# Optimization experiments

Hardware: AMD Instinct MI355X
Metric: run time of the kernel (lower is better)

Reference implementation:

```python
import jax, jax.numpy as jnp
import numpy as np

B, T, C = 32, 2048, 64
H, N = 1, 64            # head_size = n_embd -> single head of size 64 (CUDA assert: C//H == 64)
LAYER_ID, N_LAYER = 1, 4
TMIX_DIM, TDEC_DIM = 32, 64
LN_EPS = 1e-5 * 8**2


def setup_inputs() -> dict:
    key = jax.random.key(0)
    ks = jax.random.split(key, 10)
    r01 = LAYER_ID / (N_LAYER - 1)          # ratio_0_to_1
    r10 = 1.0 - LAYER_ID / N_LAYER          # ratio_1_to_almost0
    ddd = (jnp.arange(C, dtype=jnp.float32) / C)[None, None, :]   # (1,1,C)
    tm_x = 1.0 - ddd**r10
    tm_w = 1.0 - ddd**r10
    tm_k = 1.0 - ddd**r10
    tm_v = 1.0 - (ddd**r10 + 0.3 * r01)
    tm_r = 1.0 - ddd**(0.5 * r10)
    tm_g = 1.0 - ddd**(0.5 * r10)
    unif = lambda k, s: jax.random.uniform(k, s, minval=-1e-4, maxval=1e-4, dtype=jnp.float32)
    maa_w1 = unif(ks[0], (C, TMIX_DIM * 5))
    maa_w2 = unif(ks[1], (5, TMIX_DIM, C))
    n = jnp.arange(C, dtype=jnp.float32)
    t_decay = (-6.0 + 5.0 * (n / (C - 1))**(0.7 + 1.3 * r01))[None, None, :]   # (1,1,C)
    dec_w1 = unif(ks[2], (C, TDEC_DIM))
    dec_w2 = unif(ks[3], (TDEC_DIM, C))
    zig = ((n + 1) % 3 - 1) * 0.1
    u = (r01 * (1.0 - n / (C - 1)) + zig).reshape(H, N)            # time_faaaa
    wscale = 0.02
    Wr = jax.random.normal(ks[4], (C, C), jnp.float32) * wscale
    Wk = jax.random.normal(ks[5], (C, C), jnp.float32) * wscale
    Wv = jax.random.normal(ks[6], (C, C), jnp.float32) * wscale
    Wg = jax.random.normal(ks[7], (C, C), jnp.float32) * wscale
    Wo = jax.random.normal(ks[8], (C, C), jnp.float32) * wscale
    ln_w = jnp.ones((C,), jnp.float32)
    ln_b = jnp.zeros((C,), jnp.float32)
    x = jax.random.normal(ks[9], (B, T, C), jnp.float32)
    return dict(x=x, tm_x=tm_x, tm_w=tm_w, tm_k=tm_k, tm_v=tm_v, tm_r=tm_r, tm_g=tm_g,
                maa_w1=maa_w1, maa_w2=maa_w2, t_decay=t_decay, dec_w1=dec_w1, dec_w2=dec_w2,
                u=u, Wr=Wr, Wk=Wk, Wv=Wv, Wg=Wg, Wo=Wo, ln_w=ln_w, ln_b=ln_b)


def _tmix(x, tm_x, tm_w, tm_k, tm_v, tm_r, tm_g, maa_w1, maa_w2, t_decay,
          dec_w1, dec_w2, u, Wr, Wk, Wv, Wg, Wo, ln_w, ln_b):
    # token shift: xx[t] = x[t-1] - x[t], x[-1] := 0
    xx = jnp.pad(x, ((0, 0), (1, 0), (0, 0)))[:, :-1] - x
    xxx = x + xx * tm_x
    a = jnp.tanh(xxx @ maa_w1).reshape(B, T, 5, TMIX_DIM)
    mw, mk, mv, mr, mg = jnp.einsum('btfk,fkc->fbtc', a, maa_w2)
    xw = x + xx * (tm_w + mw)
    xk = x + xx * (tm_k + mk)
    xv = x + xx * (tm_v + mv)
    xr = x + xx * (tm_r + mr)
    xg = x + xx * (tm_g + mg)
    r = xr @ Wr.T
    k = xk @ Wk.T
    v = xv @ Wv.T
    g = jax.nn.silu(xg @ Wg.T)
    w = t_decay + jnp.tanh(xw @ dec_w1) @ dec_w2
    dec = jnp.exp(-jnp.exp(w))               # data-dependent per-channel decay in (0,1)

    # WKV6 recurrence, time-major (T,B,H,N)
    hm = lambda t: t.reshape(B, T, H, N).transpose(1, 0, 2, 3)
    rT, kT, vT, dT = hm(r), hm(k), hm(v), hm(dec)

    def step(S, inp):
        rt, kt, vt, dt = inp                 # each (B,H,N)
        kv = kt[..., :, None] * vt[..., None, :]            # (B,H,N,N)
        y = jnp.einsum('bhi,bhij->bhj', rt, S + u[None, :, :, None] * kv)
        S = S * dt[..., :, None] + kv
        return S, y

    S0 = jnp.zeros((B, H, N, N), x.dtype)
    _, yT = jax.lax.scan(step, S0, (rT, kT, vT, dT))
    y = yT.transpose(1, 0, 2, 3).reshape(B, T, C)

    # GroupNorm over (B*T, C) with H groups, eps = 1e-5 * 64
    yg = y.reshape(B, T, H, N)
    mu = yg.mean(-1, keepdims=True)
    var = yg.var(-1, keepdims=True)
    yn = ((yg - mu) * jax.lax.rsqrt(var + LN_EPS)).reshape(B, T, C) * ln_w + ln_b
    return (yn * g) @ Wo.T


def reference(x, tm_x, tm_w, tm_k, tm_v, tm_r, tm_g, maa_w1, maa_w2, t_decay,
              dec_w1, dec_w2, u, Wr, Wk, Wv, Wg, Wo, ln_w, ln_b):
    return _tmix(x, tm_x, tm_w, tm_k, tm_v, tm_r, tm_g, maa_w1, maa_w2, t_decay,
                 dec_w1, dec_w2, u, Wr, Wk, Wv, Wg, Wo, ln_w, ln_b)
```

## Files before the change

### kernel.cpp

```cpp
#include <hip/hip_runtime.h>

#define BB 32
#define TT 2048
#define CC 64
#define BT (BB * TT)
#define NCH 64
#define CL 32
#define GN_EPS (1e-5f * 64.f)
#define SW 36
#define SA 68

typedef short short8 __attribute__((ext_vector_type(8)));
typedef float f32x4 __attribute__((ext_vector_type(4)));

__device__ __forceinline__ float rl(float v, int lane) {
  return __uint_as_float(__builtin_amdgcn_readlane(__float_as_uint(v), lane));
}
__device__ __forceinline__ float tanh_f(float x) {
  x = fminf(fmaxf(x, -10.f), 10.f);
  const float e = __expf(2.f * x);
  return (e - 1.f) / (e + 1.f);
}

__device__ __forceinline__ unsigned short f2bf(float x) {
  unsigned int u = __float_as_uint(x);
  u += 0x7FFFu + ((u >> 16) & 1u);
  return (unsigned short)(u >> 16);
}
__device__ __forceinline__ float bf2f(unsigned short h) {
  return __uint_as_float(((unsigned int)h) << 16);
}
__device__ __forceinline__ short8 cvt8(const float4 a, const float4 b) {
  short8 h;
  h[0] = (short)f2bf(a.x); h[1] = (short)f2bf(a.y);
  h[2] = (short)f2bf(a.z); h[3] = (short)f2bf(a.w);
  h[4] = (short)f2bf(b.x); h[5] = (short)f2bf(b.y);
  h[6] = (short)f2bf(b.z); h[7] = (short)f2bf(b.w);
  return h;
}
__device__ __forceinline__ short8 ldb8(const float* __restrict__ p) {
  const float4 v0 = *reinterpret_cast<const float4*>(p);
  const float4 v1 = *reinterpret_cast<const float4*>(p + 4);
  return cvt8(v0, v1);
}
__device__ __forceinline__ short8 ldb8_lds(const float* p) {
  const float4 v0 = *reinterpret_cast<const float4*>(p);
  const float4 v1 = *reinterpret_cast<const float4*>(p + 4);
  return cvt8(v0, v1);
}
__device__ __forceinline__ void splitload(const float* p, short8& h8, short8& l8) {
  const float4 v0 = *reinterpret_cast<const float4*>(p);
  const float4 v1 = *reinterpret_cast<const float4*>(p + 4);
  const float vv[8] = {v0.x, v0.y, v0.z, v0.w, v1.x, v1.y, v1.z, v1.w};
#pragma unroll
  for (int e = 0; e < 8; ++e) {
    const unsigned short hb = f2bf(vv[e]);
    h8[e] = (short)hb;
    l8[e] = (short)f2bf(vv[e] - bf2f(hb));
  }
}
__device__ __forceinline__ f32x4 mfma3(short8 ah, short8 al, short8 bh, short8 bl, f32x4 a) {
  a = __builtin_amdgcn_mfma_f32_16x16x32_bf16(ah, bh, a, 0, 0, 0);
  a = __builtin_amdgcn_mfma_f32_16x16x32_bf16(ah, bl, a, 0, 0, 0);
  a = __builtin_amdgcn_mfma_f32_16x16x32_bf16(al, bh, a, 0, 0, 0);
  return a;
}

__global__ __launch_bounds__(256) void preT_kernel(
    const float* __restrict__ maa_w1, const float* __restrict__ maa_w2,
    const float* __restrict__ dec_w1, const float* __restrict__ dec_w2,
    float* __restrict__ w1T, float* __restrict__ w2T,
    float* __restrict__ d1T, float* __restrict__ d2T)
{
  const int t0 = blockIdx.x * 256 + threadIdx.x;
  const int stride = gridDim.x * 256;
  for (int i = t0; i < 160 * 64; i += stride) {
    const int n = i >> 6, c = i & 63;
    w1T[i] = maa_w1[c * 160 + n];
  }
  for (int i = t0; i < 5 * 64 * 32; i += stride) {
    const int f = i >> 11, rem = i & 2047, n = rem >> 5, q = rem & 31;
    w2T[i] = maa_w2[(f * 32 + q) * 64 + n];
  }
  for (int i = t0; i < 4096; i += stride) {
    const int n = i >> 6, c = i & 63;
    d1T[i] = dec_w1[c * 64 + n];
    d2T[i] = dec_w2[c * 64 + n];
  }
}

#define LDS_A 36
#define LDS_X 68
__global__ __launch_bounds__(256) void mix_mfma_kernel(
    const float* __restrict__ x,
    const float* __restrict__ tm_x, const float* __restrict__ tm_w, const float* __restrict__ tm_k,
    const float* __restrict__ tm_v, const float* __restrict__ tm_r, const float* __restrict__ tm_g,
    const float* __restrict__ w1T, const float* __restrict__ w2T,
    const float* __restrict__ d1T, const float* __restrict__ d2T,
    const float* __restrict__ t_decay,
    float* __restrict__ xk_o, float* __restrict__ xv_o,
    float* __restrict__ xr_o, float* __restrict__ xg_o,
    float* __restrict__ rkdc)
{
  __shared__ float aT[4][32][LDS_A];
  __shared__ float xT[4][32][LDS_X];
  const int lane = threadIdx.x & 63;
  const int wid = threadIdx.x >> 6;
  const int col = lane & 15, half = lane >> 4;
  const int tok0 = blockIdx.x * 128 + wid * 32;

  short8 xa[2][2];
#pragma unroll
  for (int m = 0; m < 2; ++m)
#pragma unroll
    for (int kk = 0; kk < 2; ++kk) {
      const int tok = tok0 + m * 16 + col;
      const int kb = kk * 32 + half * 8;
      const float* pc = x + (size_t)tok * CC + kb;
      const float4 c0 = *reinterpret_cast<const float4*>(pc);
      const float4 c1 = *reinterpret_cast<const float4*>(pc + 4);
      float4 p0 = {0.f, 0.f, 0.f, 0.f}, p1 = {0.f, 0.f, 0.f, 0.f};
      if ((tok & (TT - 1)) != 0) {
        p0 = *reinterpret_cast<const float4*>(pc - CC);
        p1 = *reinterpret_cast<const float4*>(pc - CC + 4);
      }
      const float4 t0 = *reinterpret_cast<const float4*>(tm_x + kb);
      const float4 t1 = *reinterpret_cast<const float4*>(tm_x + kb + 4);
      const float cv[8] = {c0.x, c0.y, c0.z, c0.w, c1.x, c1.y, c1.z, c1.w};
      const float pv[8] = {p0.x, p0.y, p0.z, p0.w, p1.x, p1.y, p1.z, p1.w};
      const float tv[8] = {t0.x, t0.y, t0.z, t0.w, t1.x, t1.y, t1.z, t1.w};
      short8 h;
#pragma unroll
      for (int e = 0; e < 8; ++e)
        h[e] = (short)f2bf(fmaf(pv[e] - cv[e], tv[e], cv[e]));
      xa[m][kk] = h;
    }

  float xcv[2][4][4], xxv[2][4][4];
#pragma unroll
  for (int m = 0; m < 2; ++m)
#pragma unroll
    for (int reg = 0; reg < 4; ++reg) {
      const int tok = tok0 + m * 16 + half * 4 + reg;
      const bool has = (tok & (TT - 1)) != 0;
#pragma unroll
      for (int nt = 0; nt < 4; ++nt) {
        const size_t o = (size_t)tok * CC + nt * 16 + col;
        const float cur = x[o];
        const float prv = has ? x[o - CC] : 0.f;
        xcv[m][nt][reg] = cur;
        xxv[m][nt][reg] = prv - cur;
      }
    }

  auto process_f = [&](int f, const float* __restrict__ tmf,
                       float* __restrict__ gout) {
    f32x4 acc1[2][2];
#pragma unroll
    for (int m = 0; m < 2; ++m)
#pragma unroll
      for (int ntf = 0; ntf < 2; ++ntf) acc1[m][ntf] = (f32x4){0.f, 0.f, 0.f, 0.f};
    short8 b1[2][2];
#pragma unroll
    for (int ntf = 0; ntf < 2; ++ntf)
#pragma unroll
      for (int kk = 0; kk < 2; ++kk)
        b1[ntf][kk] = ldb8(w1T + (size_t)(f * 32 + ntf * 16 + col) * 64 + kk * 32 + half * 8);
#pragma unroll
    for (int m = 0; m < 2; ++m)
#pragma unroll
      for (int ntf = 0; ntf < 2; ++ntf)
#pragma unroll
        for (int kk = 0; kk < 2; ++kk)
          acc1[m][ntf] = __builtin_amdgcn_mfma_f32_16x16x32_bf16(
              xa[m][kk], b1[ntf][kk], acc1[m][ntf], 0, 0, 0);
#pragma unroll
    for (int m = 0; m < 2; ++m)
#pragma unroll
      for (int ntf = 0; ntf < 2; ++ntf)
#pragma unroll
        for (int reg = 0; reg < 4; ++reg)
          aT[wid][m * 16 + half * 4 + reg][ntf * 16 + col] = tanh_f(acc1[m][ntf][reg]);
    short8 a2[2];
#pragma unroll
    for (int m = 0; m < 2; ++m)
      a2[m] = ldb8_lds(&aT[wid][m * 16 + col][half * 8]);
    f32x4 acc2[2][4];
#pragma unroll
    for (int m = 0; m < 2; ++m)
#pragma unroll
      for (int nt = 0; nt < 4; ++nt) acc2[m][nt] = (f32x4){0.f, 0.f, 0.f, 0.f};
    short8 b2[4];
#pragma unroll
    for (int nt = 0; nt < 4; ++nt)
      b2[nt] = ldb8(w2T + (size_t)f * 2048 + (nt * 16 + col) * 32 + half * 8);
#pragma unroll
    for (int m = 0; m < 2; ++m)
#pragma unroll
      for (int nt = 0; nt < 4; ++nt)
        acc2[m][nt] = __builtin_amdgcn_mfma_f32_16x16x32_bf16(
            a2[m], b2[nt], acc2[m][nt], 0, 0, 0);
    float tmf4[4];
#pragma unroll
    for (int nt = 0; nt < 4; ++nt) tmf4[nt] = tmf[nt * 16 + col];
#pragma unroll
    for (int m = 0; m < 2; ++m)
#pragma unroll
      for (int nt = 0; nt < 4; ++nt)
#pragma unroll
        for (int reg = 0; reg < 4; ++reg) {
          const float val = fmaf(xxv[m][nt][reg], tmf4[nt] + acc2[m][nt][reg],
                                 xcv[m][nt][reg]);
          if (gout)
            gout[(size_t)(tok0 + m * 16 + half * 4 + reg) * CC + nt * 16 + col] = val;
          else
            xT[wid][m * 16 + half * 4 + reg][nt * 16 + col] = val;
        }
  };

  process_f(1, tm_k, xk_o);
  process_f(2, tm_v, xv_o);
  process_f(3, tm_r, xr_o);
  process_f(4, tm_g, xg_o);
  process_f(0, tm_w, nullptr);

  short8 xwf[2][2];
#pragma unroll
  for (int m = 0; m < 2; ++m)
#pragma unroll
    for (int kk = 0; kk < 2; ++kk)
      xwf[m][kk] = ldb8_lds(&xT[wid][m * 16 + col][kk * 32 + half * 8]);
  f32x4 hcc[2][4];
#pragma unroll
  for (int m = 0; m < 2; ++m)
#pragma unroll
    for (int nt = 0; nt < 4; ++nt) hcc[m][nt] = (f32x4){0.f, 0.f, 0.f, 0.f};
  short8 bd[4][2];
#pragma unroll
  for (int nt = 0; nt < 4; ++nt)
#pragma unroll
    for (int kk = 0; kk < 2; ++kk)
      bd[nt][kk] = ldb8(d1T + (size_t)(nt * 16 + col) * 64 + kk * 32 + half * 8);
#pragma unroll
  for (int m = 0; m < 2; ++m)
#pragma unroll
    for (int nt = 0; nt < 4; ++nt)
#pragma unroll
      for (int kk = 0; kk < 2; ++kk)
        hcc[m][nt] = __builtin_amdgcn_mfma_f32_16x16x32_bf16(
            xwf[m][kk], bd[nt][kk], hcc[m][nt], 0, 0, 0);
#pragma unroll
  for (int m = 0; m < 2; ++m)
#pragma unroll
    for (int nt = 0; nt < 4; ++nt)
#pragma unroll
      for (int reg = 0; reg < 4; ++reg)
        xT[wid][m * 16 + half * 4 + reg][nt * 16 + col] = tanh_f(hcc[m][nt][reg]);
  short8 hf[2][2];
#pragma unroll
  for (int m = 0; m < 2; ++m)
#pragma unroll
    for (int kk = 0; kk < 2; ++kk)
      hf[m][kk] = ldb8_lds(&xT[wid][m * 16 + col][kk * 32 + half * 8]);
  f32x4 wfa[2][4];
#pragma unroll
  for (int m = 0; m < 2; ++m)
#pragma unroll
    for (int nt = 0; nt < 4; ++nt) wfa[m][nt] = (f32x4){0.f, 0.f, 0.f, 0.f};
#pragma unroll
  for (int nt = 0; nt < 4; ++nt)
#pragma unroll
    for (int kk = 0; kk < 2; ++kk)
      bd[nt][kk] = ldb8(d2T + (size_t)(nt * 16 + col) * 64 + kk * 32 + half * 8);
#pragma unroll
  for (int m = 0; m < 2; ++m)
#pragma unroll
    for (int nt = 0; nt < 4; ++nt)
#pragma unroll
      for (int kk = 0; kk < 2; ++kk)
        wfa[m][nt] = __builtin_amdgcn_mfma_f32_16x16x32_bf16(
            hf[m][kk], bd[nt][kk], wfa[m][nt], 0, 0, 0);
  float td4[4];
#pragma unroll
  for (int nt = 0; nt < 4; ++nt) td4[nt] = t_decay[nt * 16 + col];
#pragma unroll
  for (int m = 0; m < 2; ++m)
#pragma unroll
    for (int nt = 0; nt < 4; ++nt)
#pragma unroll
      for (int reg = 0; reg < 4; ++reg)
        rkdc[4 * ((size_t)(tok0 + m * 16 + half * 4 + reg) * CC + nt * 16 + col) + 2] =
            __expf(wfa[m][nt][reg] + td4[nt]);
}

__device__ __forceinline__ void load_afrag(
    const float* __restrict__ X, int tok0, int col, int half,
    short8 ah[2][2], short8 al[2][2])
{
#pragma unroll
  for (int m = 0; m < 2; ++m)
#pragma unroll
    for (int kk = 0; kk < 2; ++kk)
      splitload(X + (size_t)(tok0 + m * 16 + col) * CC + kk * 32 + half * 8,
                ah[m][kk], al[m][kk]);
}
__device__ __forceinline__ void load_bfrag(
    const float* __restrict__ W, int col, int half,
    short8 bh[4][2], short8 bl[4][2])
{
#pragma unroll
  for (int n = 0; n < 4; ++n)
#pragma unroll
    for (int kk = 0; kk < 2; ++kk)
      splitload(W + (size_t)(n * 16 + col) * CC + kk * 32 + half * 8,
                bh[n][kk], bl[n][kk]);
}
__device__ __forceinline__ void gemm_acc(
    const short8 ah[2][2], const short8 al[2][2],
    const short8 bh[4][2], const short8 bl[4][2], f32x4 acc[2][4])
{
#pragma unroll
  for (int m = 0; m < 2; ++m)
#pragma unroll
    for (int n = 0; n < 4; ++n) {
      f32x4 a = acc[m][n];
#pragma unroll
      for (int kk = 0; kk < 2; ++kk)
        a = mfma3(ah[m][kk], al[m][kk], bh[n][kk], bl[n][kk], a);
      acc[m][n] = a;
    }
}

__global__ __launch_bounds__(256) void proj4_mfma_kernel(
    const float* __restrict__ xk_i, const float* __restrict__ xv_i,
    const float* __restrict__ xr_i, const float* __restrict__ xg_i,
    const float* __restrict__ u,
    const float* __restrict__ Wr, const float* __restrict__ Wk, const float* __restrict__ Wv,
    const float* __restrict__ Wg,
    float* __restrict__ rkdc, float* __restrict__ v_o, float* __restrict__ g_o)
{
  const int lane = threadIdx.x & 63;
  const int wid = threadIdx.x >> 6;
  const int col = lane & 15, half = lane >> 4;
  const int tok0 = blockIdx.x * 128 + wid * 32;

  short8 ah[2][2], al[2][2], bh[4][2], bl[4][2];
  f32x4 accr[2][4], acck[2][4];

  load_bfrag(Wr, col, half, bh, bl);
  load_afrag(xr_i, tok0, col, half, ah, al);
#pragma unroll
  for (int m = 0; m < 2; ++m)
#pragma unroll
    for (int n = 0; n < 4; ++n) accr[m][n] = (f32x4){0.f, 0.f, 0.f, 0.f};
  gemm_acc(ah, al, bh, bl, accr);

  load_bfrag(Wk, col, half, bh, bl);
  load_afrag(xk_i, tok0, col, half, ah, al);
#pragma unroll
  for (int m = 0; m < 2; ++m)
#pragma unroll
    for (int n = 0; n < 4; ++n) acck[m][n] = (f32x4){0.f, 0.f, 0.f, 0.f};
  gemm_acc(ah, al, bh, bl, acck);

  float uv[4];
#pragma unroll
  for (int n = 0; n < 4; ++n) uv[n] = u[n * 16 + col];
  float ctv[2][4];
#pragma unroll
  for (int m = 0; m < 2; ++m)
#pragma unroll
    for (int reg = 0; reg < 4; ++reg) {
      float p = 0.f;
#pragma unroll
      for (int n = 0; n < 4; ++n)
        p += accr[m][n][reg] * uv[n] * acck[m][n][reg];
      p += __shfl_xor(p, 1, 64);
      p += __shfl_xor(p, 2, 64);
      p += __shfl_xor(p, 4, 64);
      p += __shfl_xor(p, 8, 64);
      ctv[m][reg] = p;
    }

#pragma unroll
  for (int m = 0; m < 2; ++m)
#pragma unroll
    for (int n = 0; n < 4; ++n)
#pragma unroll
      for (int reg = 0; reg < 4; ++reg) {
        const int token = tok0 + m * 16 + half * 4 + reg;
        const size_t o = (size_t)token * CC + n * 16 + col;
        rkdc[4 * o + 0] = accr[m][n][reg];
        rkdc[4 * o + 1] = acck[m][n][reg];
        rkdc[4 * o + 3] = ctv[m][reg];
      }

  load_bfrag(Wv, col, half, bh, bl);
  load_afrag(xv_i, tok0, col, half, ah, al);
#pragma unroll
  for (int m = 0; m < 2; ++m)
#pragma unroll
    for (int n = 0; n < 4; ++n) accr[m][n] = (f32x4){0.f, 0.f, 0.f, 0.f};
  gemm_acc(ah, al, bh, bl, accr);
#pragma unroll
  for (int m = 0; m < 2; ++m)
#pragma unroll
    for (int n = 0; n < 4; ++n)
#pragma unroll
      for (int reg = 0; reg < 4; ++reg) {
        const int token = tok0 + m * 16 + half * 4 + reg;
        v_o[(size_t)token * CC + n * 16 + col] = accr[m][n][reg];
      }

  load_bfrag(Wg, col, half, bh, bl);
  load_afrag(xg_i, tok0, col, half, ah, al);
#pragma unroll
  for (int m = 0; m < 2; ++m)
#pragma unroll
    for (int n = 0; n < 4; ++n) accr[m][n] = (f32x4){0.f, 0.f, 0.f, 0.f};
  gemm_acc(ah, al, bh, bl, accr);
#pragma unroll
  for (int m = 0; m < 2; ++m)
#pragma unroll
    for (int n = 0; n < 4; ++n)
#pragma unroll
      for (int reg = 0; reg < 4; ++reg) {
        const int token = tok0 + m * 16 + half * 4 + reg;
        const float gg = accr[m][n][reg];
        g_o[(size_t)token * CC + n * 16 + col] = gg / (1.f + __expf(-gg));
      }
}

__global__ __launch_bounds__(128) void chunkA_mfma_kernel(
    const float4* __restrict__ rkdc, const float* __restrict__ v_i,
    float* __restrict__ SlocT, float* __restrict__ Dp)
{
  __shared__ float ktS[2][64 * SW];
  __shared__ float vtS[2][64 * SW];
  __shared__ float cumS[2][64];
  const int lane = threadIdx.x & 63;
  const int w = threadIdx.x >> 6;
  const int bch = __builtin_amdgcn_readfirstlane((blockIdx.x << 1) + w);
  float* ktL = ktS[w];
  float* vtL = vtS[w];
  float* cumL = cumS[w];
  const int col = lane & 15, half = lane >> 4;

  const float4* fq = rkdc + (size_t)bch * (CL * CC) + lane;
  const float* vq = v_i + (size_t)bch * (CL * CC) + lane;

  float cum = 0.f;
  for (int t = 0; t < CL; ++t) {
    const float4 f = fq[t * CC];
    const float vv = vq[t * CC];
    cum += f.z;
    ktL[lane * SW + t] = f.y * __expf(cum);
    vtL[lane * SW + t] = vv;
  }
  cumL[lane] = cum;
  Dp[(size_t)bch * CC + lane] = __expf(-cum);

  short8 vah[4], val[4], kbh[4], kbl[4];
#pragma unroll
  for (int m = 0; m < 4; ++m)
    splitload(vtL + (m * 16 + col) * SW + half * 8, vah[m], val[m]);
#pragma unroll
  for (int n = 0; n < 4; ++n)
    splitload(ktL + (n * 16 + col) * SW + half * 8, kbh[n], kbl[n]);

  f32x4 acc[4][4];
#pragma unroll
  for (int m = 0; m < 4; ++m)
#pragma unroll
    for (int n = 0; n < 4; ++n) {
      acc[m][n] = (f32x4){0.f, 0.f, 0.f, 0.f};
      acc[m][n] = mfma3(vah[m], val[m], kbh[n], kbl[n], acc[m][n]);
    }

  float acl[4];
#pragma unroll
  for (int n = 0; n < 4; ++n) acl[n] = __expf(-cumL[n * 16 + col]);

  float* so = SlocT + (size_t)bch * (CC * CC);
#pragma unroll
  for (int m = 0; m < 4; ++m)
#pragma unroll
    for (int n = 0; n < 4; ++n)
#pragma unroll
      for (int reg = 0; reg < 4; ++reg) {
        const int jj = m * 16 + half * 4 + reg;
        const int ii = n * 16 + col;
        so[jj * CC + ii] = acc[m][n][reg] * acl[n];
      }
}

__global__ __launch_bounds__(1024) void combine_kernel(
    float* __restrict__ buf, const float* __restrict__ Dp)
{
  const int b = blockIdx.x, tid = threadIdx.x;
  __shared__ float sDp[NCH * CC];
  for (int idx = tid; idx < NCH * CC; idx += 1024)
    sDp[idx] = Dp[(size_t)b * NCH * CC + idx];
  __syncthreads();
  float run[4] = {0.f, 0.f, 0.f, 0.f};
  for (int ch = 0; ch < NCH; ++ch) {
    const size_t base = ((size_t)(b * NCH + ch)) * (CC * CC);
    const float* drow = sDp + ch * CC;
#pragma unroll
    for (int k2 = 0; k2 < 4; ++k2) {
      const int idx = tid + (k2 << 10);
      const float tmp = buf[base + idx];
      buf[base + idx] = run[k2];
      run[k2] = fmaf(run[k2], drow[idx & 63], tmp);
    }
  }
}

__global__ __launch_bounds__(128) void scanC_mfma_kernel(
    const float4* __restrict__ rkdc, const float* __restrict__ v_i,
    const float* __restrict__ S0T, const float* __restrict__ g_i,
    const float* __restrict__ ln_w, const float* __restrict__ ln_b,
    const float* __restrict__ Wo, float* __restrict__ out)
{
  __shared__ float rtS[2][32 * SA];
  __shared__ float ktS[2][32 * SA];
  __shared__ float vtS[2][64 * SW];
  __shared__ float ctS[2][CL];
  const int lane = threadIdx.x & 63;
  const int w = threadIdx.x >> 6;
  const int bch = __builtin_amdgcn_readfirstlane((blockIdx.x << 1) + w);
  float* rtL = rtS[w];
  float* ktL = ktS[w];
  float* vtL = vtS[w];
  float* ctL = ctS[w];
  const int col = lane & 15, half = lane >> 4;

  const float4* fq = rkdc + (size_t)bch * (CL * CC) + lane;
  const float* vq = v_i + (size_t)bch * (CL * CC) + lane;

  float cum = 0.f;
  for (int t = 0; t < CL; ++t) {
    const float4 f = fq[t * CC];
    const float vv = vq[t * CC];
    rtL[t * SA + lane] = f.x * __expf(-cum);
    cum += f.z;
    ktL[t * SA + lane] = f.y * __expf(cum);
    vtL[lane * SW + t] = vv;
    if (lane == 0) ctL[t] = f.w;
  }

  short8 rah[2][2], ral[2][2];
#pragma unroll
  for (int m = 0; m < 2; ++m)
#pragma unroll
    for (int kk = 0; kk < 2; ++kk)
      splitload(rtL + (m * 16 + col) * SA + kk * 32 + half * 8, rah[m][kk], ral[m][kk]);
  short8 kbh[2][2], kbl[2][2];
#pragma unroll
  for (int n = 0; n < 2; ++n)
#pragma unroll
    for (int kk = 0; kk < 2; ++kk)
      splitload(ktL + (n * 16 + col) * SA + kk * 32 + half * 8, kbh[n][kk], kbl[n][kk]);

  f32x4 pacc[2][2];
#pragma unroll
  for (int m = 0; m < 2; ++m)
#pragma unroll
    for (int n = 0; n < 2; ++n) {
      pacc[m][n] = (f32x4){0.f, 0.f, 0.f, 0.f};
#pragma unroll
      for (int kk = 0; kk < 2; ++kk)
        pacc[m][n] = mfma3(rah[m][kk], ral[m][kk], kbh[n][kk], kbl[n][kk], pacc[m][n]);
    }

#pragma unroll
  for (int m = 0; m < 2; ++m)
#pragma unroll
    for (int n = 0; n < 2; ++n)
#pragma unroll
      for (int reg = 0; reg < 4; ++reg) {
        const int tt = m * 16 + half * 4 + reg;
        const int ss = n * 16 + col;
        const float pv = (ss < tt) ? pacc[m][n][reg] : (ss == tt ? ctL[tt] : 0.f);
        ktL[tt * SA + ss] = pv;
      }

  short8 pah[2], pal[2];
#pragma unroll
  for (int m = 0; m < 2; ++m)
    splitload(ktL + (m * 16 + col) * SA + half * 8, pah[m], pal[m]);
  short8 vbh[4], vbl[4];
#pragma unroll
  for (int n = 0; n < 4; ++n)
    splitload(vtL + (n * 16 + col) * SW + half * 8, vbh[n], vbl[n]);

  f32x4 yacc[2][4];
#pragma unroll
  for (int m = 0; m < 2; ++m)
#pragma unroll
    for (int n = 0; n < 4; ++n) {
      yacc[m][n] = (f32x4){0.f, 0.f, 0.f, 0.f};
      yacc[m][n] = mfma3(pah[m], pal[m], vbh[n], vbl[n], yacc[m][n]);
    }

  const float* s0b = S0T + (size_t)bch * (CC * CC);
#pragma unroll
  for (int kk = 0; kk < 2; ++kk) {
    short8 sbh[4], sbl[4];
#pragma unroll
    for (int n = 0; n < 4; ++n)
      splitload(s0b + (size_t)(n * 16 + col) * CC + kk * 32 + half * 8, sbh[n], sbl[n]);
#pragma unroll
    for (int m = 0; m < 2; ++m)
#pragma unroll
      for (int n = 0; n < 4; ++n)
        yacc[m][n] = mfma3(rah[m][kk], ral[m][kk], sbh[n], sbl[n], yacc[m][n]);
  }

  float s1v[2][4], s2v[2][4];
#pragma unroll
  for (int m = 0; m < 2; ++m)
#pragma unroll
    for (int reg = 0; reg < 4; ++reg) {
      float a = 0.f, b2 = 0.f;
#pragma unroll
      for (int n = 0; n < 4; ++n) {
        const float y = yacc[m][n][reg];
        a += y; b2 += y * y;
      }
      a += __shfl_xor(a, 1, 64); b2 += __shfl_xor(b2, 1, 64);
      a += __shfl_xor(a, 2, 64); b2 += __shfl_xor(b2, 2, 64);
      a += __shfl_xor(a, 4, 64); b2 += __shfl_xor(b2, 4, 64);
      a += __shfl_xor(a, 8, 64); b2 += __shfl_xor(b2, 8, 64);
      s1v[m][reg] = a; s2v[m][reg] = b2;
    }

#pragma unroll
  for (int m = 0; m < 2; ++m)
#pragma unroll
    for (int n = 0; n < 4; ++n) {
      const int cj = n * 16 + col;
      const float lnw = ln_w[cj], lnb = ln_b[cj];
#pragma unroll
      for (int reg = 0; reg < 4; ++reg) {
        const int tt = m * 16 + half * 4 + reg;
        const float y = yacc[m][n][reg];
        const float mu = s1v[m][reg] * (1.f / CC);
        const float var = s2v[m][reg] * (1.f / CC) - mu * mu;
        const float z = (y - mu) * rsqrtf(var + GN_EPS) * lnw + lnb;
        const float gg = g_i[((size_t)bch * CL + tt) * CC + cj];
        rtL[tt * SA + cj] = z * gg;
      }
    }

  f32x4 oacc[2][4];
#pragma unroll
  for (int m = 0; m < 2; ++m)
#pragma unroll
    for (int n = 0; n < 4; ++n) oacc[m][n] = (f32x4){0.f, 0.f, 0.f, 0.f};
#pragma unroll
  for (int kk = 0; kk < 2; ++kk) {
    short8 zah[2], zal[2];
#pragma unroll
    for (int m = 0; m < 2; ++m)
      splitload(rtL + (m * 16 + col) * SA + kk * 32 + half * 8, zah[m], zal[m]);
    short8 wbh[4], wbl[4];
#pragma unroll
    for (int n = 0; n < 4; ++n)
      splitload(Wo + (size_t)(n * 16 + col) * CC + kk * 32 + half * 8, wbh[n], wbl[n]);
#pragma unroll
    for (int m = 0; m < 2; ++m)
#pragma unroll
      for (int n = 0; n < 4; ++n)
        oacc[m][n] = mfma3(zah[m], zal[m], wbh[n], wbl[n], oacc[m][n]);
  }

#pragma unroll
  for (int m = 0; m < 2; ++m)
#pragma unroll
    for (int n = 0; n < 4; ++n)
#pragma unroll
      for (int reg = 0; reg < 4; ++reg) {
        const int tt = m * 16 + half * 4 + reg;
        out[((size_t)bch * CL + tt) * CC + n * 16 + col] = oacc[m][n][reg];
      }
}

extern "C" void kernel_launch(void* const* d_in, const int* in_sizes, int n_in,
                              void* d_out, int out_size, void* d_ws, size_t ws_size,
                              hipStream_t stream) {
  const float* x       = (const float*)d_in[0];
  const float* tm_x    = (const float*)d_in[1];
  const float* tm_w    = (const float*)d_in[2];
  const float* tm_k    = (const float*)d_in[3];
  const float* tm_v    = (const float*)d_in[4];
  const float* tm_r    = (const float*)d_in[5];
  const float* tm_g    = (const float*)d_in[6];
  const float* maa_w1  = (const float*)d_in[7];
  const float* maa_w2  = (const float*)d_in[8];
  const float* t_decay = (const float*)d_in[9];
  const float* dec_w1  = (const float*)d_in[10];
  const float* dec_w2  = (const float*)d_in[11];
  const float* u       = (const float*)d_in[12];
  const float* Wr      = (const float*)d_in[13];
  const float* Wk      = (const float*)d_in[14];
  const float* Wv      = (const float*)d_in[15];
  const float* Wg      = (const float*)d_in[16];
  const float* Wo      = (const float*)d_in[17];
  const float* ln_w    = (const float*)d_in[18];
  const float* ln_b    = (const float*)d_in[19];

  const size_t M = (size_t)BT * CC;
  float* ws   = (float*)d_ws;
  float* xk_o = ws;
  float* xv_o = ws + M;
  float* xr_o = ws + 2 * M;
  float* xg_o = ws + 3 * M;
  float* g_o  = ws + 4 * M;
  float* v_o  = ws + 5 * M;
  float* rkdc = ws + 6 * M;
  float* scb  = ws;
  float* Dp   = ws + 2 * M;
  float* w1T  = ws + 10 * M;
  float* w2T  = w1T + 160 * 64;
  float* d1T  = w2T + 5 * 64 * 32;
  float* d2T  = d1T + 4096;
  float* out  = (float*)d_out;

  preT_kernel<<<64, 256, 0, stream>>>(
      maa_w1, maa_w2, dec_w1, dec_w2, w1T, w2T, d1T, d2T);

  mix_mfma_kernel<<<BT / 128, 256, 0, stream>>>(
      x, tm_x, tm_w, tm_k, tm_v, tm_r, tm_g,
      w1T, w2T, d1T, d2T, t_decay,
      xk_o, xv_o, xr_o, xg_o, rkdc);

  proj4_mfma_kernel<<<BT / 128, 256, 0, stream>>>(
      xk_o, xv_o, xr_o, xg_o, u, Wr, Wk, Wv, Wg, rkdc, v_o, g_o);

  chunkA_mfma_kernel<<<(BB * NCH) / 2, 128, 0, stream>>>(
      (const float4*)rkdc, v_o, scb, Dp);

  combine_kernel<<<BB, 1024, 0, stream>>>(scb, Dp);

  scanC_mfma_kernel<<<(BB * NCH) / 2, 128, 0, stream>>>(
      (const float4*)rkdc, v_o, scb, g_o, ln_w, ln_b, Wo, out);
}
```

Measured before the change: 195.2 us.

## Fuse token-mix and R/K/V/G projection kernels into one prep kernel

Merges the mix kernel and the four-projection kernel so each mixed input (xr, xk, xv, xg) stays in LDS and is fed straight into the projection GEMM, instead of being written to and reread from global memory. The decay exp is kept in registers and rkdc is written as a single float4 per element rather than scattered scalar stores. This removes about four full activation round trips through HBM and one kernel launch. In exchange the fused kernel holds more live registers (the decay values plus the accumulators), which may lower occupancy.

```diff
diff --git a/kernel.cpp b/kernel.cpp
--- a/kernel.cpp
+++ b/kernel.cpp
@@ -13,15 +13,11 @@
 typedef short short8 __attribute__((ext_vector_type(8)));
 typedef float f32x4 __attribute__((ext_vector_type(4)));
 
-__device__ __forceinline__ float rl(float v, int lane) {
-  return __uint_as_float(__builtin_amdgcn_readlane(__float_as_uint(v), lane));
-}
 __device__ __forceinline__ float tanh_f(float x) {
   x = fminf(fmaxf(x, -10.f), 10.f);
   const float e = __expf(2.f * x);
   return (e - 1.f) / (e + 1.f);
 }
-
 __device__ __forceinline__ unsigned short f2bf(float x) {
   unsigned int u = __float_as_uint(x);
   u += 0x7FFFu + ((u >> 16) & 1u);
@@ -38,12 +34,7 @@
   h[6] = (short)f2bf(b.z); h[7] = (short)f2bf(b.w);
   return h;
 }
-__device__ __forceinline__ short8 ldb8(const float* __restrict__ p) {
-  const float4 v0 = *reinterpret_cast<const float4*>(p);
-  const float4 v1 = *reinterpret_cast<const float4*>(p + 4);
-  return cvt8(v0, v1);
-}
-__device__ __forceinline__ short8 ldb8_lds(const float* p) {
+__device__ __forceinline__ short8 ldb8(const float* p) {
   const float4 v0 = *reinterpret_cast<const float4*>(p);
   const float4 v1 = *reinterpret_cast<const float4*>(p + 4);
   return cvt8(v0, v1);
@@ -91,16 +82,16 @@
 
 #define LDS_A 36
 #define LDS_X 68
-__global__ __launch_bounds__(256) void mix_mfma_kernel(
+__global__ __launch_bounds__(256) void prep_fused_kernel(
     const float* __restrict__ x,
     const float* __restrict__ tm_x, const float* __restrict__ tm_w, const float* __restrict__ tm_k,
     const float* __restrict__ tm_v, const float* __restrict__ tm_r, const float* __restrict__ tm_g,
     const float* __restrict__ w1T, const float* __restrict__ w2T,
     const float* __restrict__ d1T, const float* __restrict__ d2T,
-    const float* __restrict__ t_decay,
-    float* __restrict__ xk_o, float* __restrict__ xv_o,
-    float* __restrict__ xr_o, float* __restrict__ xg_o,
-    float* __restrict__ rkdc)
+    const float* __restrict__ t_decay, const float* __restrict__ u,
+    const float* __restrict__ Wr, const float* __restrict__ Wk,
+    const float* __restrict__ Wv, const float* __restrict__ Wg,
+    float* __restrict__ rkdc, float* __restrict__ v_o, float* __restrict__ g_o)
 {
   __shared__ float aT[4][32][LDS_A];
   __shared__ float xT[4][32][LDS_X];
@@ -153,8 +144,7 @@
       }
     }
 
-  auto process_f = [&](int f, const float* __restrict__ tmf,
-                       float* __restrict__ gout) {
+  auto mix_f = [&](int f, const float* __restrict__ tmf) {
     f32x4 acc1[2][2];
 #pragma unroll
     for (int m = 0; m < 2; ++m)
@@ -184,7 +174,7 @@
     short8 a2[2];
 #pragma unroll
     for (int m = 0; m < 2; ++m)
-      a2[m] = ldb8_lds(&aT[wid][m * 16 + col][half * 8]);
+      a2[m] = ldb8(&aT[wid][m * 16 + col][half * 8]);
     f32x4 acc2[2][4];
 #pragma unroll
     for (int m = 0; m < 2; ++m)
@@ -208,47 +198,59 @@
 #pragma unroll
       for (int nt = 0; nt < 4; ++nt)
 #pragma unroll
-        for (int reg = 0; reg < 4; ++reg) {
-          const float val = fmaf(xxv[m][nt][reg], tmf4[nt] + acc2[m][nt][reg],
-                                 xcv[m][nt][reg]);
-          if (gout)
-            gout[(size_t)(tok0 + m * 16 + half * 4 + reg) * CC + nt * 16 + col] = val;
-          else
-            xT[wid][m * 16 + half * 4 + reg][nt * 16 + col] = val;
-        }
+        for (int reg = 0; reg < 4; ++reg)
+          xT[wid][m * 16 + half * 4 + reg][nt * 16 + col] =
+              fmaf(xxv[m][nt][reg], tmf4[nt] + acc2[m][nt][reg], xcv[m][nt][reg]);
   };
-
-  process_f(1, tm_k, xk_o);
-  process_f(2, tm_v, xv_o);
-  process_f(3, tm_r, xr_o);
-  process_f(4, tm_g, xg_o);
-  process_f(0, tm_w, nullptr);
-
-  short8 xwf[2][2];
+  auto xT_afrag = [&](short8 ah[2][2], short8 al[2][2]) {
+#pragma unroll
+    for (int m = 0; m < 2; ++m)
+#pragma unroll
+      for (int kk = 0; kk < 2; ++kk)
+        splitload(&xT[wid][m * 16 + col][kk * 32 + half * 8], ah[m][kk], al[m][kk]);
+  };
+  auto proj_gemm = [&](const float* __restrict__ W, const short8 ah[2][2],
+                       const short8 al[2][2], f32x4 acc[2][4]) {
+#pragma unroll
+    for (int m = 0; m < 2; ++m)
+#pragma unroll
+      for (int n = 0; n < 4; ++n) acc[m][n] = (f32x4){0.f, 0.f, 0.f, 0.f};
+#pragma unroll
+    for (int n = 0; n < 4; ++n)
+#pragma unroll
+      for (int kk = 0; kk < 2; ++kk) {
+        short8 bh, bl;
+        splitload(W + (size_t)(n * 16 + col) * CC + kk * 32 + half * 8, bh, bl);
+#pragma unroll
+        for (int m = 0; m < 2; ++m)
+          acc[m][n] = mfma3(ah[m][kk], al[m][kk], bh, bl, acc[m][n]);
+      }
+  };
+
+  short8 ah[2][2], al[2][2];
+
+  mix_f(0, tm_w);
+  short8 xwh[2][2];
 #pragma unroll
   for (int m = 0; m < 2; ++m)
 #pragma unroll
     for (int kk = 0; kk < 2; ++kk)
-      xwf[m][kk] = ldb8_lds(&xT[wid][m * 16 + col][kk * 32 + half * 8]);
+      xwh[m][kk] = ldb8(&xT[wid][m * 16 + col][kk * 32 + half * 8]);
   f32x4 hcc[2][4];
 #pragma unroll
   for (int m = 0; m < 2; ++m)
 #pragma unroll
     for (int nt = 0; nt < 4; ++nt) hcc[m][nt] = (f32x4){0.f, 0.f, 0.f, 0.f};
-  short8 bd[4][2];
 #pragma unroll
   for (int nt = 0; nt < 4; ++nt)
 #pragma unroll
-    for (int kk = 0; kk < 2; ++kk)
-      bd[nt][kk] = ldb8(d1T + (size_t)(nt * 16 + col) * 64 + kk * 32 + half * 8);
-#pragma unroll
-  for (int m = 0; m < 2; ++m)
-#pragma unroll
-    for (int nt = 0; nt < 4; ++nt)
-#pragma unroll
-      for (int kk = 0; kk < 2; ++kk)
+    for (int kk = 0; kk < 2; ++kk) {
+      const short8 bd = ldb8(d1T + (size_t)(nt * 16 + col) * 64 + kk * 32 + half * 8);
+#pragma unroll
+      for (int m = 0; m < 2; ++m)
         hcc[m][nt] = __builtin_amdgcn_mfma_f32_16x16x32_bf16(
-            xwf[m][kk], bd[nt][kk], hcc[m][nt], 0, 0, 0);
+            xwh[m][kk], bd, hcc[m][nt], 0, 0, 0);
+    }
 #pragma unroll
   for (int m = 0; m < 2; ++m)
 #pragma unroll
@@ -256,12 +258,11 @@
 #pragma unroll
       for (int reg = 0; reg < 4; ++reg)
         xT[wid][m * 16 + half * 4 + reg][nt * 16 + col] = tanh_f(hcc[m][nt][reg]);
-  short8 hf[2][2];
 #pragma unroll
   for (int m = 0; m < 2; ++m)
 #pragma unroll
     for (int kk = 0; kk < 2; ++kk)
-      hf[m][kk] = ldb8_lds(&xT[wid][m * 16 + col][kk * 32 + half * 8]);
+      xwh[m][kk] = ldb8(&xT[wid][m * 16 + col][kk * 32 + half * 8]);
   f32x4 wfa[2][4];
 #pragma unroll
   for (int m = 0; m < 2; ++m)
@@ -270,105 +271,43 @@
 #pragma unroll
   for (int nt = 0; nt < 4; ++nt)
 #pragma unroll
-    for (int kk = 0; kk < 2; ++kk)
-      bd[nt][kk] = ldb8(d2T + (size_t)(nt * 16 + col) * 64 + kk * 32 + half * 8);
-#pragma unroll
-  for (int m = 0; m < 2; ++m)
-#pragma unroll
-    for (int nt = 0; nt < 4; ++nt)
-#pragma unroll
-      for (int kk = 0; kk < 2; ++kk)
+    for (int kk = 0; kk < 2; ++kk) {
+      const short8 bd = ldb8(d2T + (size_t)(nt * 16 + col) * 64 + kk * 32 + half * 8);
+#pragma unroll
+      for (int m = 0; m < 2; ++m)
         wfa[m][nt] = __builtin_amdgcn_mfma_f32_16x16x32_bf16(
-            hf[m][kk], bd[nt][kk], wfa[m][nt], 0, 0, 0);
-  float td4[4];
-#pragma unroll
-  for (int nt = 0; nt < 4; ++nt) td4[nt] = t_decay[nt * 16 + col];
-#pragma unroll
-  for (int m = 0; m < 2; ++m)
-#pragma unroll
-    for (int nt = 0; nt < 4; ++nt)
-#pragma unroll
-      for (int reg = 0; reg < 4; ++reg)
-        rkdc[4 * ((size_t)(tok0 + m * 16 + half * 4 + reg) * CC + nt * 16 + col) + 2] =
-            __expf(wfa[m][nt][reg] + td4[nt]);
-}
-
-__device__ __forceinline__ void load_afrag(
-    const float* __restrict__ X, int tok0, int col, int half,
-    short8 ah[2][2], short8 al[2][2])
-{
-#pragma unroll
-  for (int m = 0; m < 2; ++m)
-#pragma unroll
-    for (int kk = 0; kk < 2; ++kk)
-      splitload(X + (size_t)(tok0 + m * 16 + col) * CC + kk * 32 + half * 8,
-                ah[m][kk], al[m][kk]);
-}
-__device__ __forceinline__ void load_bfrag(
-    const float* __restrict__ W, int col, int half,
-    short8 bh[4][2], short8 bl[4][2])
-{
-#pragma unroll
-  for (int n = 0; n < 4; ++n)
-#pragma unroll
-    for (int kk = 0; kk < 2; ++kk)
-      splitload(W + (size_t)(n * 16 + col) * CC + kk * 32 + half * 8,
-                bh[n][kk], bl[n][kk]);
-}
-__device__ __forceinline__ void gemm_acc(
-    const short8 ah[2][2], const short8 al[2][2],
-    const short8 bh[4][2], const short8 bl[4][2], f32x4 acc[2][4])
-{
-#pragma unroll
-  for (int m = 0; m < 2; ++m)
-#pragma unroll
-    for (int n = 0; n < 4; ++n) {
-      f32x4 a = acc[m][n];
-#pragma unroll
-      for (int kk = 0; kk < 2; ++kk)
-        a = mfma3(ah[m][kk], al[m][kk], bh[n][kk], bl[n][kk], a);
-      acc[m][n] = a;
-    }
-}
-
-__global__ __launch_bounds__(256) void proj4_mfma_kernel(
-    const float* __restrict__ xk_i, const float* __restrict__ xv_i,
-    const float* __restrict__ xr_i, const float* __restrict__ xg_i,
-    const float* __restrict__ u,
-    const float* __restrict__ Wr, const float* __restrict__ Wk, const float* __restrict__ Wv,
-    const float* __restrict__ Wg,
-    float* __restrict__ rkdc, float* __restrict__ v_o, float* __restrict__ g_o)
-{
-  const int lane = threadIdx.x & 63;
-  const int wid = threadIdx.x >> 6;
-  const int col = lane & 15, half = lane >> 4;
-  const int tok0 = blockIdx.x * 128 + wid * 32;
-
-  short8 ah[2][2], al[2][2], bh[4][2], bl[4][2];
-  f32x4 accr[2][4], acck[2][4];
-
-  load_bfrag(Wr, col, half, bh, bl);
-  load_afrag(xr_i, tok0, col, half, ah, al);
-#pragma unroll
-  for (int m = 0; m < 2; ++m)
-#pragma unroll
-    for (int n = 0; n < 4; ++n) accr[m][n] = (f32x4){0.f, 0.f, 0.f, 0.f};
-  gemm_acc(ah, al, bh, bl, accr);
-
-  load_bfrag(Wk, col, half, bh, bl);
-  load_afrag(xk_i, tok0, col, half, ah, al);
-#pragma unroll
-  for (int m = 0; m < 2; ++m)
-#pragma unroll
-    for (int n = 0; n < 4; ++n) acck[m][n] = (f32x4){0.f, 0.f, 0.f, 0.f};
-  gemm_acc(ah, al, bh, bl, acck);
+            xwh[m][kk], bd, wfa[m][nt], 0, 0, 0);
+    }
+  float ewv[2][4][4];
+  {
+    float td4[4];
+#pragma unroll
+    for (int nt = 0; nt < 4; ++nt) td4[nt] = t_decay[nt * 16 + col];
+#pragma unroll
+    for (int m = 0; m < 2; ++m)
+#pragma unroll
+      for (int nt = 0; nt < 4; ++nt)
+#pragma unroll
+        for (int reg = 0; reg < 4; ++reg)
+          ewv[m][nt][reg] = __expf(wfa[m][nt][reg] + td4[nt]);
+  }
+
+  mix_f(3, tm_r);
+  xT_afrag(ah, al);
+  f32x4 accr[2][4];
+  proj_gemm(Wr, ah, al, accr);
+
+  mix_f(1, tm_k);
+  xT_afrag(ah, al);
+  f32x4 acck[2][4];
+  proj_gemm(Wk, ah, al, acck);
 
   float uv[4];
 #pragma unroll
   for (int n = 0; n < 4; ++n) uv[n] = u[n * 16 + col];
-  float ctv[2][4];
-#pragma unroll
-  for (int m = 0; m < 2; ++m)
+#pragma unroll
+  for (int m = 0; m < 2; ++m) {
+    float ctv[4];
 #pragma unroll
     for (int reg = 0; reg < 4; ++reg) {
       float p = 0.f;
@@ -379,29 +318,22 @@
       p += __shfl_xor(p, 2, 64);
       p += __shfl_xor(p, 4, 64);
       p += __shfl_xor(p, 8, 64);
-      ctv[m][reg] = p;
-    }
-
-#pragma unroll
-  for (int m = 0; m < 2; ++m)
+      ctv[reg] = p;
+    }
 #pragma unroll
     for (int n = 0; n < 4; ++n)
 #pragma unroll
       for (int reg = 0; reg < 4; ++reg) {
         const int token = tok0 + m * 16 + half * 4 + reg;
         const size_t o = (size_t)token * CC + n * 16 + col;
-        rkdc[4 * o + 0] = accr[m][n][reg];
-        rkdc[4 * o + 1] = acck[m][n][reg];
-        rkdc[4 * o + 3] = ctv[m][reg];
-      }
-
-  load_bfrag(Wv, col, half, bh, bl);
-  load_afrag(xv_i, tok0, col, half, ah, al);
-#pragma unroll
-  for (int m = 0; m < 2; ++m)
-#pragma unroll
-    for (int n = 0; n < 4; ++n) accr[m][n] = (f32x4){0.f, 0.f, 0.f, 0.f};
-  gemm_acc(ah, al, bh, bl, accr);
+        *reinterpret_cast<float4*>(rkdc + 4 * o) =
+            make_float4(accr[m][n][reg], acck[m][n][reg], ewv[m][n][reg], ctv[reg]);
+      }
+  }
+
+  mix_f(2, tm_v);
+  xT_afrag(ah, al);
+  proj_gemm(Wv, ah, al, accr);
 #pragma unroll
   for (int m = 0; m < 2; ++m)
 #pragma unroll
@@ -412,13 +344,9 @@
         v_o[(size_t)token * CC + n * 16 + col] = accr[m][n][reg];
       }
 
-  load_bfrag(Wg, col, half, bh, bl);
-  load_afrag(xg_i, tok0, col, half, ah, al);
-#pragma unroll
-  for (int m = 0; m < 2; ++m)
-#pragma unroll
-    for (int n = 0; n < 4; ++n) accr[m][n] = (f32x4){0.f, 0.f, 0.f, 0.f};
-  gemm_acc(ah, al, bh, bl, accr);
+  mix_f(4, tm_g);
+  xT_afrag(ah, al);
+  proj_gemm(Wg, ah, al, accr);
 #pragma unroll
   for (int m = 0; m < 2; ++m)
 #pragma unroll
@@ -712,10 +640,6 @@
 
   const size_t M = (size_t)BT * CC;
   float* ws   = (float*)d_ws;
-  float* xk_o = ws;
-  float* xv_o = ws + M;
-  float* xr_o = ws + 2 * M;
-  float* xg_o = ws + 3 * M;
   float* g_o  = ws + 4 * M;
   float* v_o  = ws + 5 * M;
   float* rkdc = ws + 6 * M;
@@ -730,13 +654,10 @@
   preT_kernel<<<64, 256, 0, stream>>>(
       maa_w1, maa_w2, dec_w1, dec_w2, w1T, w2T, d1T, d2T);
 
-  mix_mfma_kernel<<<BT / 128, 256, 0, stream>>>(
+  prep_fused_kernel<<<BT / 128, 256, 0, stream>>>(
       x, tm_x, tm_w, tm_k, tm_v, tm_r, tm_g,
-      w1T, w2T, d1T, d2T, t_decay,
-      xk_o, xv_o, xr_o, xg_o, rkdc);
-
-  proj4_mfma_kernel<<<BT / 128, 256, 0, stream>>>(
-      xk_o, xv_o, xr_o, xg_o, u, Wr, Wk, Wv, Wg, rkdc, v_o, g_o);
+      w1T, w2T, d1T, d2T, t_decay, u,
+      Wr, Wk, Wv, Wg, rkdc, v_o, g_o);
 
   chunkA_mfma_kernel<<<(BB * NCH) / 2, 128, 0, stream>>>(
       (const float4*)rkdc, v_o, scb, Dp);
```

Result: faster. 171.2 us (-12.3%).
